# Performance work log

Hardware: AMD Instinct MI355X
Metric: run time of the kernel (lower is better)

## Reference

```python
import jax, jax.numpy as jnp
import numpy as np

BN_EPS = 1e-5

def batchnorm(x, gamma, beta):
    # torch BatchNorm1d training mode: biased variance over batch dim
    mean = x.mean(axis=0)
    var = x.var(axis=0)
    return (x - mean) / jnp.sqrt(var + BN_EPS) * gamma + beta

def setup_inputs() -> dict:
    key = jax.random.key(0)
    ks = jax.random.split(key, 24)
    B, N, H, F, O = 2, 4096, 64, 64, 128   # F = feature_dim; GAT dim = 2F
    s = 0.02
    inp = {}
    inp['x'] = jax.random.normal(ks[0], (B, N, N), jnp.float32)
    inp['y'] = jax.random.normal(ks[1], (B, N), jnp.float32)
    inp['adj'] = jax.random.randint(ks[2], (N, N), 0, 2, jnp.int32)
    # PreGAT segment branch
    inp['W1_seg'] = jax.random.normal(ks[3], (N, H), jnp.float32) * s
    inp['b1_seg'] = jnp.zeros((H,), jnp.float32)
    inp['g1_seg'] = jnp.ones((N * H,), jnp.float32)
    inp['bt1_seg'] = jnp.zeros((N * H,), jnp.float32)
    inp['W2_seg'] = jax.random.normal(ks[4], (H, F), jnp.float32) * s
    inp['b2_seg'] = jnp.zeros((F,), jnp.float32)
    inp['g2_seg'] = jnp.ones((N * F,), jnp.float32)
    inp['bt2_seg'] = jnp.zeros((N * F,), jnp.float32)
    # PreGAT speed branch
    inp['W1_sp'] = jax.random.normal(ks[5], (N, H), jnp.float32) * s
    inp['b1_sp'] = jnp.zeros((H,), jnp.float32)
    inp['g1_sp'] = jnp.ones((H,), jnp.float32)
    inp['bt1_sp'] = jnp.zeros((H,), jnp.float32)
    inp['W2_sp'] = jax.random.normal(ks[6], (H, F), jnp.float32) * s
    inp['b2_sp'] = jnp.zeros((F,), jnp.float32)
    inp['g2_sp'] = jnp.ones((F,), jnp.float32)
    inp['bt2_sp'] = jnp.zeros((F,), jnp.float32)
    # GAT (feature dim = 2F)
    inp['Wg1'] = jax.random.normal(ks[7], (2 * F, 2 * F), jnp.float32) * s
    inp['Wg2'] = jax.random.normal(ks[8], (2 * F, O), jnp.float32) * s
    inp['a_vec'] = jax.random.normal(ks[9], (4 * F,), jnp.float32) * s
    # AfterGAT
    inp['Wd'] = jax.random.normal(ks[10], (O, 1), jnp.float32) * s
    inp['bd'] = jnp.zeros((1,), jnp.float32)
    return inp

def reference(x, y, adj, W1_seg, b1_seg, g1_seg, bt1_seg, W2_seg, b2_seg, g2_seg, bt2_seg,
              W1_sp, b1_sp, g1_sp, bt1_sp, W2_sp, b2_sp, g2_sp, bt2_sp,
              Wg1, Wg2, a_vec, Wd, bd):
    B, N = x.shape[0], x.shape[1]
    # ---- PreGAT segment branch ----
    xs = x @ W1_seg + b1_seg                                   # [B,N,H]
    xs = batchnorm(xs.reshape(B, -1), g1_seg, bt1_seg).reshape(B, N, -1)
    xs = jax.nn.elu(xs)
    xs = xs @ W2_seg + b2_seg                                  # [B,N,F]
    xs = batchnorm(xs.reshape(B, -1), g2_seg, bt2_seg).reshape(B, N, -1)
    xs = jax.nn.elu(xs)
    # ---- PreGAT speed branch ----
    ys = y @ W1_sp + b1_sp                                     # [B,H]
    ys = jax.nn.elu(batchnorm(ys, g1_sp, bt1_sp))
    ys = ys @ W2_sp + b2_sp                                    # [B,F]
    ys = jax.nn.elu(batchnorm(ys, g2_sp, bt2_sp))
    h = jnp.concatenate([xs, jnp.broadcast_to(ys[:, None, :], (B, N, ys.shape[-1]))], axis=-1)  # [B,N,2F]
    # ---- GAT ----
    g = h @ Wg1                                                # [B,N,2F]
    F2 = g.shape[-1]
    a1, a2 = a_vec[:F2], a_vec[F2:]
    si = g @ a1                                                # [B,N] score of target i
    sj = g @ a2                                                # [B,N] score of source j
    e = jax.nn.leaky_relu(si[:, :, None] + sj[:, None, :], negative_slope=0.2)  # [B,N,N]
    mask = adj != 0                                            # [N,N]
    row_has = mask.any(axis=-1)                                # [N]
    e = jnp.where(mask[None], e, -jnp.inf)
    att = jax.nn.softmax(e, axis=-1)
    att = jnp.where((mask & row_has[:, None])[None], att, 0.0)  # zero for non-edges / empty rows
    hp = jnp.einsum('bij,bjd->bid', att, g)                    # segment-softmax + scatter-add, dense form
    hp = jax.nn.relu(hp @ Wg2)                                 # [B,N,O]
    # ---- AfterGAT ----
    out = hp @ Wd + bd                                         # [B,N,1]
    return out / (1.0 + jnp.abs(out)) - 1.0                    # softsign - 1
```

## Files before the change

kernel.cpp:

```cpp
#include <hip/hip_runtime.h>
#include <hip/hip_bf16.h>
#include <cmath>

#define NN 4096

typedef __attribute__((ext_vector_type(8))) short bf16x8;
typedef __attribute__((ext_vector_type(4))) float f32x4;

static __device__ __forceinline__ short f2bf(float f) {
  unsigned u = __float_as_uint(f);
  unsigned r = (u + 0x7FFFu + ((u >> 16) & 1u)) >> 16;
  return (short)r;
}
static __device__ __forceinline__ float bf2f(short b) {
  return __uint_as_float(((unsigned)(unsigned short)b) << 16);
}

__global__ __launch_bounds__(256) void gemm1_kernel(const float* __restrict__ X,
    const float* __restrict__ W, const float* __restrict__ bias, float* __restrict__ out) {
  __shared__ float As[64][34];
  __shared__ float Bs[64][64];
  int tid = threadIdx.x;
  int m0 = blockIdx.x * 32;
  int tx = tid & 15, ty = tid >> 4;
  float acc[2][4] = {};
  int lr = tid >> 3;
  int lk = (tid & 7) * 8;
  for (int k0 = 0; k0 < 4096; k0 += 64) {
    const float4* pa = (const float4*)(X + (size_t)(m0 + lr) * 4096 + k0 + lk);
    float4 v0 = pa[0], v1 = pa[1];
    As[lk+0][lr]=v0.x; As[lk+1][lr]=v0.y; As[lk+2][lr]=v0.z; As[lk+3][lr]=v0.w;
    As[lk+4][lr]=v1.x; As[lk+5][lr]=v1.y; As[lk+6][lr]=v1.z; As[lk+7][lr]=v1.w;
    #pragma unroll
    for (int e = 0; e < 16; ++e) {
      int idx = e * 256 + tid;
      Bs[idx >> 6][idx & 63] = W[(size_t)k0 * 64 + idx];
    }
    __syncthreads();
    #pragma unroll
    for (int kk = 0; kk < 64; ++kk) {
      float a0 = As[kk][ty*2+0], a1 = As[kk][ty*2+1];
      const float4 bv = *(const float4*)&Bs[kk][tx*4];
      acc[0][0] += a0*bv.x; acc[0][1] += a0*bv.y; acc[0][2] += a0*bv.z; acc[0][3] += a0*bv.w;
      acc[1][0] += a1*bv.x; acc[1][1] += a1*bv.y; acc[1][2] += a1*bv.z; acc[1][3] += a1*bv.w;
    }
    __syncthreads();
  }
  #pragma unroll
  for (int rr = 0; rr < 2; ++rr)
    #pragma unroll
    for (int cc = 0; cc < 4; ++cc)
      out[(size_t)(m0 + ty*2 + rr)*64 + tx*4 + cc] = acc[rr][cc] + bias[tx*4+cc];
}

__global__ void bn_elu_kernel(const float* __restrict__ src, float* __restrict__ dst,
    const float* __restrict__ gamma, const float* __restrict__ beta, int NH) {
  int idx = blockIdx.x * blockDim.x + threadIdx.x;
  if (idx >= NH) return;
  float a = src[idx], b = src[NH + idx];
  float d = 0.5f * (a - b);
  float inv = 1.0f / sqrtf(d*d + 1e-5f);
  float gm = gamma[idx], bt = beta[idx];
  float na =  d * inv * gm + bt;
  float nb = -d * inv * gm + bt;
  dst[idx]      = na > 0.f ? na : expm1f(na);
  dst[NH + idx] = nb > 0.f ? nb : expm1f(nb);
}

__global__ __launch_bounds__(256) void gemm2_kernel(const float* __restrict__ X,
    const float* __restrict__ W, const float* __restrict__ bias, float* __restrict__ out) {
  __shared__ float As[64][65];
  __shared__ float Bs[64][64];
  int tid = threadIdx.x;
  int m0 = blockIdx.x * 64;
  #pragma unroll
  for (int e = 0; e < 16; ++e) {
    int idx = e*256 + tid;
    int r = idx >> 6, c = idx & 63;
    As[r][c] = X[(size_t)m0*64 + idx];
    Bs[r][c] = W[idx];
  }
  __syncthreads();
  int tx = tid & 15, ty = tid >> 4;
  float acc[4][4] = {};
  #pragma unroll 8
  for (int kk = 0; kk < 64; ++kk) {
    float a0 = As[ty*4+0][kk], a1 = As[ty*4+1][kk], a2 = As[ty*4+2][kk], a3 = As[ty*4+3][kk];
    const float4 bv = *(const float4*)&Bs[kk][tx*4];
    acc[0][0]+=a0*bv.x; acc[0][1]+=a0*bv.y; acc[0][2]+=a0*bv.z; acc[0][3]+=a0*bv.w;
    acc[1][0]+=a1*bv.x; acc[1][1]+=a1*bv.y; acc[1][2]+=a1*bv.z; acc[1][3]+=a1*bv.w;
    acc[2][0]+=a2*bv.x; acc[2][1]+=a2*bv.y; acc[2][2]+=a2*bv.z; acc[2][3]+=a2*bv.w;
    acc[3][0]+=a3*bv.x; acc[3][1]+=a3*bv.y; acc[3][2]+=a3*bv.z; acc[3][3]+=a3*bv.w;
  }
  #pragma unroll
  for (int rr = 0; rr < 4; ++rr)
    #pragma unroll
    for (int cc = 0; cc < 4; ++cc)
      out[(size_t)(m0 + ty*4 + rr)*64 + tx*4 + cc] = acc[rr][cc] + bias[tx*4+cc];
}

__global__ __launch_bounds__(256) void gemm3_kernel(const float* __restrict__ X,
    const float* __restrict__ Wg1, const float* __restrict__ cvec, float* __restrict__ out) {
  __shared__ float As[64][65];
  __shared__ float Bs[64][128];
  int tid = threadIdx.x;
  int m0 = blockIdx.x * 64;
  int b = m0 >> 12;
  #pragma unroll
  for (int e = 0; e < 16; ++e) {
    int idx = e*256 + tid;
    As[idx>>6][idx&63] = X[(size_t)m0*64 + idx];
  }
  #pragma unroll
  for (int e = 0; e < 32; ++e) {
    int idx = e*256 + tid;
    Bs[idx>>7][idx&127] = Wg1[idx];
  }
  __syncthreads();
  int tx = tid & 15, ty = tid >> 4;
  float acc0[4][4] = {};
  float acc1[4][4] = {};
  #pragma unroll 4
  for (int kk = 0; kk < 64; ++kk) {
    float a[4];
    #pragma unroll
    for (int rr = 0; rr < 4; ++rr) a[rr] = As[ty*4+rr][kk];
    const float4 b0 = *(const float4*)&Bs[kk][tx*4];
    const float4 b1 = *(const float4*)&Bs[kk][64 + tx*4];
    #pragma unroll
    for (int rr = 0; rr < 4; ++rr) {
      acc0[rr][0]+=a[rr]*b0.x; acc0[rr][1]+=a[rr]*b0.y; acc0[rr][2]+=a[rr]*b0.z; acc0[rr][3]+=a[rr]*b0.w;
      acc1[rr][0]+=a[rr]*b1.x; acc1[rr][1]+=a[rr]*b1.y; acc1[rr][2]+=a[rr]*b1.z; acc1[rr][3]+=a[rr]*b1.w;
    }
  }
  #pragma unroll
  for (int rr = 0; rr < 4; ++rr) {
    size_t rb = (size_t)(m0 + ty*4 + rr) * 128;
    #pragma unroll
    for (int cc = 0; cc < 4; ++cc) {
      int c0 = tx*4 + cc, c1 = 64 + tx*4 + cc;
      out[rb + c0] = acc0[rr][cc] + cvec[b*128 + c0];
      out[rb + c1] = acc1[rr][cc] + cvec[b*128 + c1];
    }
  }
}

__global__ __launch_bounds__(256) void transpose_g_kernel(const float* __restrict__ g,
    short* __restrict__ gT) {
  int b = blockIdx.y;
  int j0 = blockIdx.x * 64;
  __shared__ short t[128][72];
  int tid = threadIdx.x;
  int jj = tid >> 5;
  int d0 = (tid & 31) * 4;
  #pragma unroll
  for (int r = 0; r < 8; ++r) {
    int j = jj + r * 8;
    float4 v = *(const float4*)(g + ((size_t)b*NN + j0 + j)*128 + d0);
    t[d0+0][j] = f2bf(v.x); t[d0+1][j] = f2bf(v.y);
    t[d0+2][j] = f2bf(v.z); t[d0+3][j] = f2bf(v.w);
  }
  __syncthreads();
  int d = tid >> 1, jh = (tid & 1) * 32;
  #pragma unroll
  for (int q = 0; q < 4; ++q) {
    bf16x8 v = *(const bf16x8*)&t[d][jh + q*8];
    *(bf16x8*)(gT + ((size_t)b << 19) + (size_t)d*NN + j0 + jh + q*8) = v;
  }
}

__global__ __launch_bounds__(256) void sisj_kernel(const float* __restrict__ g,
    const float* __restrict__ a_vec, float* __restrict__ si, float* __restrict__ sj) {
  int wave = threadIdx.x >> 6, lane = threadIdx.x & 63;
  int row = blockIdx.x * 4 + wave;
  const float* gr = g + (size_t)row * 128;
  float g0 = gr[lane], g1 = gr[lane + 64];
  float v1 = g0 * a_vec[lane]       + g1 * a_vec[lane + 64];
  float v2 = g0 * a_vec[128 + lane] + g1 * a_vec[192 + lane];
  #pragma unroll
  for (int off = 32; off > 0; off >>= 1) {
    v1 += __shfl_down(v1, off);
    v2 += __shfl_down(v2, off);
  }
  if (lane == 0) { si[row] = v1; sj[row] = v2; }
}

__global__ __launch_bounds__(256) void sp1_kernel(const float* __restrict__ y,
    const float* __restrict__ W, const float* __restrict__ bias, float* __restrict__ ys1) {
  int b = blockIdx.x >> 6, h = blockIdx.x & 63;
  float s = 0.f;
  for (int k = threadIdx.x; k < NN; k += 256)
    s += y[b*NN + k] * W[(size_t)k*64 + h];
  __shared__ float red[256];
  red[threadIdx.x] = s; __syncthreads();
  for (int st = 128; st > 0; st >>= 1) {
    if (threadIdx.x < st) red[threadIdx.x] += red[threadIdx.x + st];
    __syncthreads();
  }
  if (threadIdx.x == 0) ys1[blockIdx.x] = red[0] + bias[h];
}

__global__ __launch_bounds__(256) void sp2_kernel(const float* __restrict__ ys1,
    const float* __restrict__ g1, const float* __restrict__ bt1,
    const float* __restrict__ W2, const float* __restrict__ b2,
    const float* __restrict__ g2, const float* __restrict__ bt2,
    const float* __restrict__ Wg1, float* __restrict__ cvec) {
  __shared__ float e1[2][64];
  __shared__ float y2[2][64];
  __shared__ float e2[2][64];
  int tid = threadIdx.x;
  if (tid < 64) {
    float a = ys1[tid], b = ys1[64 + tid];
    float d = 0.5f * (a - b);
    float inv = 1.0f / sqrtf(d*d + 1e-5f);
    float na =  d*inv*g1[tid] + bt1[tid];
    float nb = -d*inv*g1[tid] + bt1[tid];
    e1[0][tid] = na > 0.f ? na : expm1f(na);
    e1[1][tid] = nb > 0.f ? nb : expm1f(nb);
  }
  __syncthreads();
  if (tid < 128) {
    int b = tid >> 6, h = tid & 63;
    float s = b2[h];
    for (int k = 0; k < 64; ++k) s += e1[b][k] * W2[k*64 + h];
    y2[b][h] = s;
  }
  __syncthreads();
  if (tid < 64) {
    float a = y2[0][tid], b = y2[1][tid];
    float d = 0.5f * (a - b);
    float inv = 1.0f / sqrtf(d*d + 1e-5f);
    float na =  d*inv*g2[tid] + bt2[tid];
    float nb = -d*inv*g2[tid] + bt2[tid];
    e2[0][tid] = na > 0.f ? na : expm1f(na);
    e2[1][tid] = nb > 0.f ? nb : expm1f(nb);
  }
  __syncthreads();
  {
    int b = tid >> 7, o = tid & 127;
    float s = 0.f;
    for (int h = 0; h < 64; ++h) s += e2[b][h] * Wg1[(64 + h)*128 + o];
    cvec[tid] = s;
  }
}

__global__ __launch_bounds__(256) void att_mfma_kernel(const int* __restrict__ adj,
    const float* __restrict__ si, const float* __restrict__ sj,
    const short* __restrict__ gT, float* __restrict__ hp) {
  __shared__ short w_lds[16 * 136];
  __shared__ float zinv_s[16];
  const int b = blockIdx.y;
  const int i0 = blockIdx.x * 16;
  const int tid = threadIdx.x;

  const int row = tid >> 4;
  const int jb = (tid & 15) * 8;
  const float siv = si[(size_t)b*NN + i0 + row];
  const int* arow = adj + (size_t)(i0 + row) * NN + jb;
  const float* sjrow = sj + (size_t)b * NN + jb;
  short* wrow = w_lds + row * 136 + jb;
  float zacc = 0.f;

  const int l = tid & 63, wq = tid >> 6;
  const int col = l & 15;
  const int kg = l >> 4;
  const short* apA = w_lds + col * 136 + kg * 8;
  const short* gb0 = gT + ((size_t)b << 19) + (size_t)(wq * 32 + col) * NN + kg * 8;
  const short* gb1 = gb0 + (size_t)16 * NN;
  f32x4 acc0 = {0.f, 0.f, 0.f, 0.f};
  f32x4 acc1 = {0.f, 0.f, 0.f, 0.f};

  for (int j0 = 0; j0 < NN; j0 += 128) {
    int4 a0 = *(const int4*)(arow + j0);
    int4 a1 = *(const int4*)(arow + j0 + 4);
    float4 s0 = *(const float4*)(sjrow + j0);
    float4 s1 = *(const float4*)(sjrow + j0 + 4);
    int av[8] = {a0.x, a0.y, a0.z, a0.w, a1.x, a1.y, a1.z, a1.w};
    float sv[8] = {s0.x, s0.y, s0.z, s0.w, s1.x, s1.y, s1.z, s1.w};
    bf16x8 wv;
    #pragma unroll
    for (int e = 0; e < 8; ++e) {
      float ev = siv + sv[e];
      ev = ev >= 0.f ? ev : 0.2f * ev;
      float wf = __expf(ev);
      short wb = (av[e] != 0) ? f2bf(wf) : (short)0;
      wv[e] = wb;
      zacc += bf2f(wb);
    }
    *(bf16x8*)wrow = wv;
    __syncthreads();

    #pragma unroll
    for (int kh = 0; kh < 4; ++kh) {
      bf16x8 af = *(const bf16x8*)(apA + kh * 32);
      bf16x8 bf0 = *(const bf16x8*)(gb0 + j0 + kh * 32);
      bf16x8 bf1 = *(const bf16x8*)(gb1 + j0 + kh * 32);
      acc0 = __builtin_amdgcn_mfma_f32_16x16x32_bf16(af, bf0, acc0, 0, 0, 0);
      acc1 = __builtin_amdgcn_mfma_f32_16x16x32_bf16(af, bf1, acc1, 0, 0, 0);
    }
    __syncthreads();
  }

  float z = zacc;
  z += __shfl_xor(z, 1); z += __shfl_xor(z, 2);
  z += __shfl_xor(z, 4); z += __shfl_xor(z, 8);
  if ((tid & 15) == 0) zinv_s[row] = z > 0.f ? 1.f / z : 0.f;
  __syncthreads();

  #pragma unroll
  for (int e = 0; e < 4; ++e) {
    int r = kg * 4 + e;
    float iz = zinv_s[r];
    float* o = hp + ((size_t)b*NN + i0 + r) * 128;
    o[wq * 32 + col]      = acc0[e] * iz;
    o[wq * 32 + 16 + col] = acc1[e] * iz;
  }
}

__global__ __launch_bounds__(128) void final_kernel(const float* __restrict__ hp,
    const float* __restrict__ Wg2, const float* __restrict__ Wd,
    const float* __restrict__ bd, float* __restrict__ out) {
  int row = blockIdx.x;
  int d = threadIdx.x;
  __shared__ float hrow[128];
  __shared__ float red[128];
  hrow[d] = hp[(size_t)row*128 + d];
  __syncthreads();
  float s = 0.f;
  #pragma unroll 8
  for (int k = 0; k < 128; ++k) s += hrow[k] * Wg2[(size_t)k*128 + d];
  s = s > 0.f ? s : 0.f;
  red[d] = s * Wd[d];
  __syncthreads();
  for (int st = 64; st > 0; st >>= 1) {
    if (d < st) red[d] += red[d + st];
    __syncthreads();
  }
  if (d == 0) {
    float o = red[0] + bd[0];
    out[row] = o / (1.f + fabsf(o)) - 1.f;
  }
}

extern "C" void kernel_launch(void* const* d_in, const int* in_sizes, int n_in,
                              void* d_out, int out_size, void* d_ws, size_t ws_size,
                              hipStream_t stream) {
  const float* x       = (const float*)d_in[0];
  const float* y       = (const float*)d_in[1];
  const int*   adj     = (const int*)  d_in[2];
  const float* W1_seg  = (const float*)d_in[3];
  const float* b1_seg  = (const float*)d_in[4];
  const float* g1_seg  = (const float*)d_in[5];
  const float* bt1_seg = (const float*)d_in[6];
  const float* W2_seg  = (const float*)d_in[7];
  const float* b2_seg  = (const float*)d_in[8];
  const float* g2_seg  = (const float*)d_in[9];
  const float* bt2_seg = (const float*)d_in[10];
  const float* W1_sp   = (const float*)d_in[11];
  const float* b1_sp   = (const float*)d_in[12];
  const float* g1_sp   = (const float*)d_in[13];
  const float* bt1_sp  = (const float*)d_in[14];
  const float* W2_sp   = (const float*)d_in[15];
  const float* b2_sp   = (const float*)d_in[16];
  const float* g2_sp   = (const float*)d_in[17];
  const float* bt2_sp  = (const float*)d_in[18];
  const float* Wg1     = (const float*)d_in[19];
  const float* Wg2     = (const float*)d_in[20];
  const float* a_vec   = (const float*)d_in[21];
  const float* Wd      = (const float*)d_in[22];
  const float* bd      = (const float*)d_in[23];
  float* out = (float*)d_out;

  float* ws    = (float*)d_ws;
  float* xs1   = ws;
  float* xs2   = ws + 524288;
  float* gbuf  = ws + 1048576;
  float* hpbuf = ws + 2097152;
  float* sibuf = ws + 3145728;
  float* sjbuf = ws + 3153920;
  float* ys1   = ws + 3162112;
  float* cvec  = ws + 3162240;
  short* gTbuf = (short*)(ws + 3162496);

  gemm1_kernel<<<256, 256, 0, stream>>>(x, W1_seg, b1_seg, xs1);
  bn_elu_kernel<<<1024, 256, 0, stream>>>(xs1, xs1, g1_seg, bt1_seg, 262144);
  gemm2_kernel<<<128, 256, 0, stream>>>(xs1, W2_seg, b2_seg, xs2);
  bn_elu_kernel<<<1024, 256, 0, stream>>>(xs2, xs2, g2_seg, bt2_seg, 262144);
  sp1_kernel<<<128, 256, 0, stream>>>(y, W1_sp, b1_sp, ys1);
  sp2_kernel<<<1, 256, 0, stream>>>(ys1, g1_sp, bt1_sp, W2_sp, b2_sp, g2_sp, bt2_sp, Wg1, cvec);
  gemm3_kernel<<<128, 256, 0, stream>>>(xs2, Wg1, cvec, gbuf);
  transpose_g_kernel<<<dim3(64, 2), 256, 0, stream>>>(gbuf, gTbuf);
  sisj_kernel<<<2048, 256, 0, stream>>>(gbuf, a_vec, sibuf, sjbuf);
  att_mfma_kernel<<<dim3(256, 2), 256, 0, stream>>>(adj, sibuf, sjbuf, gTbuf, hpbuf);
  final_kernel<<<8192, 128, 0, stream>>>(hpbuf, Wg2, Wd, bd, out);
}
```

Before: 485.9 us.

## Replace FP32 first GEMM with bf16 MFMA kernel using pretransposed weights

The scalar FP32 shared-memory GEMM for x @ W1_seg is replaced by a bf16 MFMA kernel. A new prep kernel converts W1_seg to bf16 and transposes it so each wave can load its B fragments directly from global memory, while X tiles are converted to bf16 and staged in LDS. This removes the FP32 FMA bottleneck on a 32M-element input read, at the cost of bf16 rounding in a 4096-long reduction and one extra small launch.

```diff
diff --git a/kernel.cpp b/kernel.cpp
--- a/kernel.cpp
+++ b/kernel.cpp
@@ -16,41 +16,62 @@
   return __uint_as_float(((unsigned)(unsigned short)b) << 16);
 }
 
-__global__ __launch_bounds__(256) void gemm1_kernel(const float* __restrict__ X,
-    const float* __restrict__ W, const float* __restrict__ bias, float* __restrict__ out) {
-  __shared__ float As[64][34];
-  __shared__ float Bs[64][64];
-  int tid = threadIdx.x;
-  int m0 = blockIdx.x * 32;
-  int tx = tid & 15, ty = tid >> 4;
-  float acc[2][4] = {};
-  int lr = tid >> 3;
-  int lk = (tid & 7) * 8;
-  for (int k0 = 0; k0 < 4096; k0 += 64) {
-    const float4* pa = (const float4*)(X + (size_t)(m0 + lr) * 4096 + k0 + lk);
-    float4 v0 = pa[0], v1 = pa[1];
-    As[lk+0][lr]=v0.x; As[lk+1][lr]=v0.y; As[lk+2][lr]=v0.z; As[lk+3][lr]=v0.w;
-    As[lk+4][lr]=v1.x; As[lk+5][lr]=v1.y; As[lk+6][lr]=v1.z; As[lk+7][lr]=v1.w;
-    #pragma unroll
-    for (int e = 0; e < 16; ++e) {
-      int idx = e * 256 + tid;
-      Bs[idx >> 6][idx & 63] = W[(size_t)k0 * 64 + idx];
+__global__ __launch_bounds__(256) void prep_w1_kernel(const float* __restrict__ W,
+    short* __restrict__ WT) {
+  __shared__ short t[64][72];
+  int k0 = blockIdx.x * 64;
+  int tid = threadIdx.x;
+  #pragma unroll
+  for (int e = 0; e < 4; ++e) {
+    int idx = e * 1024 + tid * 4;
+    int r = idx >> 6, c = idx & 63;
+    float4 v = *(const float4*)(W + (size_t)(k0 + r) * 64 + c);
+    t[c + 0][r] = f2bf(v.x); t[c + 1][r] = f2bf(v.y);
+    t[c + 2][r] = f2bf(v.z); t[c + 3][r] = f2bf(v.w);
+  }
+  __syncthreads();
+  int c = tid >> 2, kq = (tid & 3) * 16;
+  #pragma unroll
+  for (int q = 0; q < 2; ++q) {
+    bf16x8 v = *(const bf16x8*)&t[c][kq + q * 8];
+    *(bf16x8*)(WT + (size_t)c * 4096 + k0 + kq + q * 8) = v;
+  }
+}
+
+__global__ __launch_bounds__(256) void gemm1_mfma_kernel(const float* __restrict__ X,
+    const short* __restrict__ WT, const float* __restrict__ bias, float* __restrict__ out) {
+  __shared__ short As[16 * 136];
+  int tid = threadIdx.x;
+  int m0 = blockIdx.x * 16;
+  int lr = tid >> 4, lc = (tid & 15) * 8;
+  const float* xp = X + (size_t)(m0 + lr) * 4096 + lc;
+  short* wp = As + lr * 136 + lc;
+  int l = tid & 63, wq = tid >> 6;
+  int col = l & 15, kg = l >> 4;
+  const short* bp = WT + (size_t)(wq * 16 + col) * 4096 + kg * 8;
+  const short* ap = As + col * 136 + kg * 8;
+  f32x4 acc = {0.f, 0.f, 0.f, 0.f};
+  for (int k0 = 0; k0 < 4096; k0 += 128) {
+    float4 v0 = *(const float4*)(xp + k0);
+    float4 v1 = *(const float4*)(xp + k0 + 4);
+    bf16x8 wv;
+    wv[0] = f2bf(v0.x); wv[1] = f2bf(v0.y); wv[2] = f2bf(v0.z); wv[3] = f2bf(v0.w);
+    wv[4] = f2bf(v1.x); wv[5] = f2bf(v1.y); wv[6] = f2bf(v1.z); wv[7] = f2bf(v1.w);
+    *(bf16x8*)wp = wv;
+    __syncthreads();
+    #pragma unroll
+    for (int ks = 0; ks < 4; ++ks) {
+      bf16x8 af = *(const bf16x8*)(ap + ks * 32);
+      bf16x8 bf = *(const bf16x8*)(bp + k0 + ks * 32);
+      acc = __builtin_amdgcn_mfma_f32_16x16x32_bf16(af, bf, acc, 0, 0, 0);
     }
     __syncthreads();
-    #pragma unroll
-    for (int kk = 0; kk < 64; ++kk) {
-      float a0 = As[kk][ty*2+0], a1 = As[kk][ty*2+1];
-      const float4 bv = *(const float4*)&Bs[kk][tx*4];
-      acc[0][0] += a0*bv.x; acc[0][1] += a0*bv.y; acc[0][2] += a0*bv.z; acc[0][3] += a0*bv.w;
-      acc[1][0] += a1*bv.x; acc[1][1] += a1*bv.y; acc[1][2] += a1*bv.z; acc[1][3] += a1*bv.w;
-    }
-    __syncthreads();
-  }
-  #pragma unroll
-  for (int rr = 0; rr < 2; ++rr)
-    #pragma unroll
-    for (int cc = 0; cc < 4; ++cc)
-      out[(size_t)(m0 + ty*2 + rr)*64 + tx*4 + cc] = acc[rr][cc] + bias[tx*4+cc];
+  }
+  #pragma unroll
+  for (int e = 0; e < 4; ++e) {
+    int r = kg * 4 + e;
+    out[(size_t)(m0 + r) * 64 + wq * 16 + col] = acc[e] + bias[wq * 16 + col];
+  }
 }
 
 __global__ void bn_elu_kernel(const float* __restrict__ src, float* __restrict__ dst,
@@ -381,8 +402,10 @@
   float* ys1   = ws + 3162112;
   float* cvec  = ws + 3162240;
   short* gTbuf = (short*)(ws + 3162496);
-
-  gemm1_kernel<<<256, 256, 0, stream>>>(x, W1_seg, b1_seg, xs1);
+  short* w1T   = (short*)(ws + 3686784);
+
+  prep_w1_kernel<<<64, 256, 0, stream>>>(W1_seg, w1T);
+  gemm1_mfma_kernel<<<512, 256, 0, stream>>>(x, w1T, b1_seg, xs1);
   bn_elu_kernel<<<1024, 256, 0, stream>>>(xs1, xs1, g1_seg, bt1_seg, 262144);
   gemm2_kernel<<<128, 256, 0, stream>>>(xs1, W2_seg, b2_seg, xs2);
   bn_elu_kernel<<<1024, 256, 0, stream>>>(xs2, xs2, g2_seg, bt2_seg, 262144);
```

Result: faster. 403.5 us (-17.0%).
